# Kernel optimization log

Hardware: AMD Instinct MI355X
Metric: run time of the kernel (lower is better)

The kernel has to match this reference:

```python
import jax, jax.numpy as jnp
import numpy as np

K = 20  # rec list length

def _isin(a, b, bmask=None):
    # membership of each element of a in (masked) b; a,b are small [K] int arrays
    eq = a[:, None] == b[None, :]
    if bmask is not None:
        eq = eq & bmask[None, :]
    return eq.any(axis=1)

def _compact(vals, mask):
    # stable compaction of masked elements to the front, preserving order
    n = vals.shape[0]
    order = jnp.argsort(jnp.where(mask, jnp.arange(n), n))
    return vals[order], mask.sum()

def _fuse_one(top, mid, sim, probs, key):
    # greedy set-intersection fusion of three K-length rec lists (mirrors __fuse_rec_lists)
    m_tm = _isin(top, mid)
    m_ts = _isin(top, sim)
    m_ms = _isin(mid, sim)
    # faithful to the torch code's elementwise AND of masks over different lists
    mask_common = m_tm & m_ts & m_ms
    in_common_mid = _isin(mid, top, mask_common)
    mask_tm = m_tm & ~mask_common
    mask_ts = m_ts & ~mask_common
    mask_ms = m_ms & ~in_common_mid
    top_pool_m = ~mask_common & ~mask_tm & ~mask_ts
    mid_pool_m = ~in_common_mid & ~_isin(mid, top, mask_tm) & ~mask_ms
    sim_pool_m = (~_isin(sim, top, mask_common) & ~_isin(sim, top, mask_ts)
                  & ~_isin(sim, mid, mask_ms))
    det_vals = jnp.concatenate([top, top, top, mid])          # [4K]
    det_mask = jnp.concatenate([mask_common, mask_tm, mask_ts, mask_ms])
    det, n_det = _compact(det_vals, det_mask)
    pools, counts = jax.vmap(_compact)(
        jnp.stack([top, mid, sim]),
        jnp.stack([top_pool_m, mid_pool_m, sim_pool_m]))      # [3,K], [3]
    logp = jnp.log(probs)

    def step(carry, t):
        ptr, key = carry
        key, sub = jax.random.split(key)
        avail = ptr < counts
        idx = jax.random.categorical(sub, jnp.where(avail, logp, -jnp.inf))
        sampled = pools[idx, jnp.minimum(ptr[idx], K - 1)]
        use_det = t < n_det
        val = jnp.where(use_det, det[t], sampled)
        ptr = ptr.at[idx].add(jnp.where(use_det, 0, 1))
        return (ptr, key), val

    _, out = jax.lax.scan(step, (jnp.zeros(3, jnp.int32), key), jnp.arange(K))
    return out

def setup_inputs() -> dict:
    key = jax.random.key(0)
    ks = jax.random.split(key, 9)
    B, p_dim, latent = 2048, 64, 128
    n_users, n_items = 2000, 20000
    n_top, n_mid = 2000, 5000
    rng = np.random.default_rng(0)
    perm = rng.permutation(n_items)
    return {
        "X": jax.random.normal(ks[0], (B, p_dim), jnp.float32),
        "W_sp": jax.random.normal(ks[1], (p_dim, latent), jnp.float32) * 0.1,
        "W_sd": jax.random.normal(ks[2], (latent, n_top), jnp.float32) * 0.1,
        "W_mp": jax.random.normal(ks[3], (p_dim, latent), jnp.float32) * 0.1,
        "W_md": jax.random.normal(ks[4], (latent, n_mid), jnp.float32) * 0.1,
        "W_mapper": jax.random.normal(ks[5], (p_dim, 3), jnp.float32) * 0.1,
        "user_ratings": jax.random.uniform(ks[6], (n_users, n_items), jnp.float32),
        "user_personalities": jax.random.normal(ks[7], (n_users, p_dim), jnp.float32),
        "top_map": jnp.asarray(perm[:n_top], jnp.int32),
        "mid_map": jnp.asarray(perm[n_top:n_top + n_mid], jnp.int32),
    }

def reference(X, W_sp, W_sd, W_mp, W_md, W_mapper, user_ratings,
              user_personalities, top_map, mid_map):
    B = X.shape[0]
    n_items = user_ratings.shape[1]
    # small decoder path: prior -> dec -> scatter into full item space
    top_sub = (X @ W_sp) @ W_sd                                  # [B, n_top]
    top_full = jnp.zeros((B, n_items), X.dtype).at[:, top_map].set(top_sub)
    mid_sub = (X @ W_mp) @ W_md                                  # [B, n_mid]
    mid_full = jnp.zeros((B, n_items), X.dtype).at[:, mid_map].set(mid_sub)
    # personality-similarity recommendations
    sim_scores = (X @ user_personalities.T) @ user_ratings       # [B, n_items]
    top_idx = jax.lax.top_k(top_full, K)[1].astype(jnp.int32)
    mid_idx = jax.lax.top_k(mid_full, K)[1].astype(jnp.int32)
    sim_idx = jax.lax.top_k(sim_scores, K)[1].astype(jnp.int32)
    probs = jax.nn.softmax(X @ W_mapper, axis=-1)                # [B, 3]
    keys = jax.random.split(jax.random.key(42), B)
    out = jax.vmap(_fuse_one)(top_idx, mid_idx, sim_idx, probs, keys)
    return out.astype(jnp.float32)                               # [B, K]
```

## Files before the change

kernel.cpp:

```cpp
#include <hip/hip_runtime.h>
#include <stdint.h>
#include <math.h>

#define KK 20
#define RNG_PARTITIONABLE 1


__device__ __forceinline__ void tf2x32(uint32_t k0, uint32_t k1,
                                       uint32_t c0, uint32_t c1,
                                       uint32_t& o0, uint32_t& o1) {
  const uint32_t ks2 = k0 ^ k1 ^ 0x1BD11BDAu;
  uint32_t x0 = c0 + k0, x1 = c1 + k1;
#define ROTL32(x,d) (((x) << (d)) | ((x) >> (32 - (d))))
#define R4(ra,rb,rc,rd) \
  x0 += x1; x1 = ROTL32(x1, ra); x1 ^= x0; \
  x0 += x1; x1 = ROTL32(x1, rb); x1 ^= x0; \
  x0 += x1; x1 = ROTL32(x1, rc); x1 ^= x0; \
  x0 += x1; x1 = ROTL32(x1, rd); x1 ^= x0;
  R4(13,15,26,6);  x0 += k1;  x1 += ks2 + 1u;
  R4(17,29,16,24); x0 += ks2; x1 += k0 + 2u;
  R4(13,15,26,6);  x0 += k0;  x1 += k1 + 3u;
  R4(17,29,16,24); x0 += k1;  x1 += ks2 + 4u;
  R4(13,15,26,6);  x0 += ks2; x1 += k0 + 5u;
  o0 = x0; o1 = x1;
#undef R4
#undef ROTL32
}

__device__ __forceinline__ float u01_from_bits(uint32_t b) {
  float f = __uint_as_float((b >> 9) | 0x3f800000u) - 1.0f;
  return (f == 0.0f) ? 1.17549435e-38f : f;
}

#define GK 16

__global__ __launch_bounds__(256) void gemm_nn_k(
    const float* __restrict__ A, int lda,
    const float* __restrict__ Bg, int ldb,
    float* __restrict__ C, int ldc,
    int M, int N, int K, int kc) {
  __shared__ __align__(16) float As[GK][64 + 4];
  __shared__ __align__(16) float Bs[GK][128 + 4];
  const int tid = threadIdx.x;
  const int row0 = blockIdx.y * 64;
  const int col0 = blockIdx.x * 128;
  const int tr = tid >> 4, tc = tid & 15;
  const int kc_eff = (kc > 0) ? kc : K;
  float accM[4][8];
#pragma unroll
  for (int i = 0; i < 4; ++i)
#pragma unroll
    for (int j = 0; j < 8; ++j) accM[i][j] = 0.f;

  for (int c0 = 0; c0 < K; c0 += kc_eff) {
    const int kend = (c0 + kc_eff < K) ? (c0 + kc_eff) : K;
    float acc[4][8];
#pragma unroll
    for (int i = 0; i < 4; ++i)
#pragma unroll
      for (int j = 0; j < 8; ++j) acc[i][j] = 0.f;

    for (int k0 = c0; k0 < kend; k0 += GK) {
      {
        int ar = tid >> 2, ac = (tid & 3) << 2;
        int gr = row0 + ar, gc = k0 + ac;
        float4 v = make_float4(0.f, 0.f, 0.f, 0.f);
        if (gr < M) {
          if (gc + 3 < K) v = *(const float4*)(A + (size_t)gr * lda + gc);
          else {
            float t0 = (gc     < K) ? A[(size_t)gr * lda + gc]     : 0.f;
            float t1 = (gc + 1 < K) ? A[(size_t)gr * lda + gc + 1] : 0.f;
            float t2 = (gc + 2 < K) ? A[(size_t)gr * lda + gc + 2] : 0.f;
            float t3 = (gc + 3 < K) ? A[(size_t)gr * lda + gc + 3] : 0.f;
            v = make_float4(t0, t1, t2, t3);
          }
        }
        As[ac + 0][ar] = v.x; As[ac + 1][ar] = v.y;
        As[ac + 2][ar] = v.z; As[ac + 3][ar] = v.w;
      }
#pragma unroll
      for (int i = 0; i < 2; ++i) {
        int s = tid + i * 256;
        int br = s >> 5, bc = (s & 31) << 2;
        int gk = k0 + br, gc = col0 + bc;
        float4 v = make_float4(0.f, 0.f, 0.f, 0.f);
        if (gk < K) {
          if (gc + 3 < N) v = *(const float4*)(Bg + (size_t)gk * ldb + gc);
          else {
            float t0 = (gc     < N) ? Bg[(size_t)gk * ldb + gc]     : 0.f;
            float t1 = (gc + 1 < N) ? Bg[(size_t)gk * ldb + gc + 1] : 0.f;
            float t2 = (gc + 2 < N) ? Bg[(size_t)gk * ldb + gc + 2] : 0.f;
            float t3 = (gc + 3 < N) ? Bg[(size_t)gk * ldb + gc + 3] : 0.f;
            v = make_float4(t0, t1, t2, t3);
          }
        }
        *(float4*)&Bs[br][bc] = v;
      }
      __syncthreads();
#pragma unroll
      for (int kk = 0; kk < GK; ++kk) {
        float4 av = *(const float4*)&As[kk][tr << 2];
        float4 b0 = *(const float4*)&Bs[kk][tc << 2];
        float4 b1 = *(const float4*)&Bs[kk][64 + (tc << 2)];
        float a[4] = {av.x, av.y, av.z, av.w};
        float b[8] = {b0.x, b0.y, b0.z, b0.w, b1.x, b1.y, b1.z, b1.w};
#pragma unroll
        for (int i = 0; i < 4; ++i)
#pragma unroll
          for (int j = 0; j < 8; ++j)
            acc[i][j] = __fadd_rn(acc[i][j], __fmul_rn(a[i], b[j]));
      }
      __syncthreads();
    }
#pragma unroll
    for (int i = 0; i < 4; ++i)
#pragma unroll
      for (int j = 0; j < 8; ++j) accM[i][j] = __fadd_rn(accM[i][j], acc[i][j]);
  }
#pragma unroll
  for (int i = 0; i < 4; ++i) {
    int gr = row0 + (tr << 2) + i;
    if (gr >= M) continue;
#pragma unroll
    for (int j = 0; j < 8; ++j) {
      int gc = col0 + ((j < 4) ? (tc << 2) + j : 64 + (tc << 2) + (j - 4));
      if (gc < N) C[(size_t)gr * ldc + gc] = accM[i][j];
    }
  }
}

__global__ __launch_bounds__(256) void gemm_nt_k(
    const float* __restrict__ A, int lda,
    const float* __restrict__ Bg, int ldb,
    float* __restrict__ C, int ldc,
    int M, int N, int K) {
  __shared__ __align__(16) float As[16][128 + 4];
  __shared__ __align__(16) float Bs[16][128 + 4];
  const int tid = threadIdx.x;
  const int row0 = blockIdx.y * 128;
  const int col0 = blockIdx.x * 128;
  const int tr = tid >> 4, tc = tid & 15;
  float acc[8][8];
#pragma unroll
  for (int i = 0; i < 8; ++i)
#pragma unroll
    for (int j = 0; j < 8; ++j) acc[i][j] = 0.f;

  for (int k0 = 0; k0 < K; k0 += 16) {
#pragma unroll
    for (int i = 0; i < 2; ++i) {
      int s = tid + i * 256;
      int ar = s >> 2, ac = (s & 3) << 2;
      int gr = row0 + ar, gc = k0 + ac;
      float4 v = make_float4(0.f, 0.f, 0.f, 0.f);
      if (gr < M) {
        if (gc + 3 < K) v = *(const float4*)(A + (size_t)gr * lda + gc);
        else {
          float t0 = (gc     < K) ? A[(size_t)gr * lda + gc]     : 0.f;
          float t1 = (gc + 1 < K) ? A[(size_t)gr * lda + gc + 1] : 0.f;
          float t2 = (gc + 2 < K) ? A[(size_t)gr * lda + gc + 2] : 0.f;
          float t3 = (gc + 3 < K) ? A[(size_t)gr * lda + gc + 3] : 0.f;
          v = make_float4(t0, t1, t2, t3);
        }
      }
      As[ac + 0][ar] = v.x; As[ac + 1][ar] = v.y;
      As[ac + 2][ar] = v.z; As[ac + 3][ar] = v.w;
    }
#pragma unroll
    for (int i = 0; i < 2; ++i) {
      int s = tid + i * 256;
      int nr = s >> 2, kcc = (s & 3) << 2;
      int gn = col0 + nr, gk = k0 + kcc;
      float4 v = make_float4(0.f, 0.f, 0.f, 0.f);
      if (gn < N) {
        if (gk + 3 < K) v = *(const float4*)(Bg + (size_t)gn * ldb + gk);
        else {
          float t0 = (gk     < K) ? Bg[(size_t)gn * ldb + gk]     : 0.f;
          float t1 = (gk + 1 < K) ? Bg[(size_t)gn * ldb + gk + 1] : 0.f;
          float t2 = (gk + 2 < K) ? Bg[(size_t)gn * ldb + gk + 2] : 0.f;
          float t3 = (gk + 3 < K) ? Bg[(size_t)gn * ldb + gk + 3] : 0.f;
          v = make_float4(t0, t1, t2, t3);
        }
      }
      Bs[kcc + 0][nr] = v.x; Bs[kcc + 1][nr] = v.y;
      Bs[kcc + 2][nr] = v.z; Bs[kcc + 3][nr] = v.w;
    }
    __syncthreads();
#pragma unroll
    for (int kk = 0; kk < 16; ++kk) {
      float4 a0 = *(const float4*)&As[kk][tr * 8];
      float4 a1 = *(const float4*)&As[kk][tr * 8 + 4];
      float4 b0 = *(const float4*)&Bs[kk][tc * 8];
      float4 b1 = *(const float4*)&Bs[kk][tc * 8 + 4];
      float a[8] = {a0.x, a0.y, a0.z, a0.w, a1.x, a1.y, a1.z, a1.w};
      float b[8] = {b0.x, b0.y, b0.z, b0.w, b1.x, b1.y, b1.z, b1.w};
#pragma unroll
      for (int i = 0; i < 8; ++i)
#pragma unroll
        for (int j = 0; j < 8; ++j)
          acc[i][j] = __fadd_rn(acc[i][j], __fmul_rn(a[i], b[j]));
    }
    __syncthreads();
  }
#pragma unroll
  for (int i = 0; i < 8; ++i) {
    int gr = row0 + tr * 8 + i;
    if (gr >= M) continue;
#pragma unroll
    for (int j = 0; j < 8; ++j) {
      int gc = col0 + tc * 8 + j;
      if (gc < N) C[(size_t)gr * ldc + gc] = acc[i][j];
    }
  }
}

__global__ __launch_bounds__(256) void topk20_k(
    const float* __restrict__ mat, int ld, int ncols, int col_off,
    const int* __restrict__ map,
    float* __restrict__ sval, int* __restrict__ sidx, int merge) {
  __shared__ float shv[256][KK];
  __shared__ int   shi[256][KK];
  __shared__ float ov[KK];
  __shared__ int   oi[KK];
  const int r = blockIdx.x, t = threadIdx.x;
  const float* __restrict__ row = mat + (size_t)r * ld;
  float lv[KK]; int li[KK];
#pragma unroll
  for (int i = 0; i < KK; ++i) { lv[i] = -INFINITY; li[i] = 0x7fffffff; }
  for (int c = t; c < ncols; c += 256) {
    float v = row[c];
    if (v > lv[KK - 1]) {
      float cv = v; int ci = c;
#pragma unroll
      for (int i = 0; i < KK; ++i) {
        bool sw = cv > lv[i];
        float tv = lv[i]; int ti = li[i];
        lv[i] = sw ? cv : tv; li[i] = sw ? ci : ti;
        cv = sw ? tv : cv;    ci = sw ? ti : ci;
      }
    }
  }
#pragma unroll
  for (int i = 0; i < KK; ++i) { shv[t][i] = lv[i]; shi[t][i] = li[i]; }
  __syncthreads();
  if (t < 64) {
    int hp0 = 0, hp1 = 0, hp2 = 0, hp3 = 0;
    for (int round = 0; round < KK; ++round) {
      int base = t * 4;
      float v0 = (hp0 < KK) ? shv[base + 0][hp0] : -INFINITY;
      int   i0 = (hp0 < KK) ? shi[base + 0][hp0] : 0x7fffffff;
      float v1 = (hp1 < KK) ? shv[base + 1][hp1] : -INFINITY;
      int   i1 = (hp1 < KK) ? shi[base + 1][hp1] : 0x7fffffff;
      float v2 = (hp2 < KK) ? shv[base + 2][hp2] : -INFINITY;
      int   i2 = (hp2 < KK) ? shi[base + 2][hp2] : 0x7fffffff;
      float v3 = (hp3 < KK) ? shv[base + 3][hp3] : -INFINITY;
      int   i3 = (hp3 < KK) ? shi[base + 3][hp3] : 0x7fffffff;
      float bv = v0; int bi = i0; int bq = 0;
      if (v1 > bv || (v1 == bv && i1 < bi)) { bv = v1; bi = i1; bq = 1; }
      if (v2 > bv || (v2 == bv && i2 < bi)) { bv = v2; bi = i2; bq = 2; }
      if (v3 > bv || (v3 == bv && i3 < bi)) { bv = v3; bi = i3; bq = 3; }
      float cv = bv; int ci = bi; int cl = t; int cq = bq;
#pragma unroll
      for (int s2 = 1; s2 < 64; s2 <<= 1) {
        float vx = __shfl_xor(cv, s2);
        int   ix = __shfl_xor(ci, s2);
        int   lx = __shfl_xor(cl, s2);
        int   qx = __shfl_xor(cq, s2);
        if (vx > cv || (vx == cv && ix < ci)) { cv = vx; ci = ix; cl = lx; cq = qx; }
      }
      if (t == 0) { ov[round] = cv; oi[round] = ci; }
      if (cl == t) { hp0 += (cq == 0); hp1 += (cq == 1); hp2 += (cq == 2); hp3 += (cq == 3); }
    }
    if (t == 0) {
      float* SV = sval + (size_t)r * KK;
      int*   SI = sidx + (size_t)r * KK;
      if (!merge) {
        for (int i = 0; i < KK; ++i) {
          SV[i] = ov[i];
          SI[i] = map ? map[oi[i]] : (oi[i] + col_off);
        }
      } else {
        float mv[KK]; int mi[KK];
        int a = 0, b = 0;
        for (int i = 0; i < KK; ++i) {
          float va = SV[a]; int ia = SI[a];
          float vb = ov[b]; int ib = oi[b] + col_off;
          bool ta = (va > vb) || (va == vb && ia < ib);
          if (ta) { mv[i] = va; mi[i] = ia; ++a; }
          else    { mv[i] = vb; mi[i] = ib; ++b; }
        }
        for (int i = 0; i < KK; ++i) { SV[i] = mv[i]; SI[i] = mi[i]; }
      }
    }
  }
}

__global__ __launch_bounds__(256) void fuse_k(
    const float* __restrict__ X, const float* __restrict__ Wmap,
    const int* __restrict__ siT, const int* __restrict__ siM,
    const int* __restrict__ siS, float* __restrict__ out, int B) {
  int r = blockIdx.x * blockDim.x + threadIdx.x;
  if (r >= B) return;
  int top[KK], mid[KK], sim[KK];
  for (int i = 0; i < KK; ++i) {
    top[i] = siT[(size_t)r * KK + i];
    mid[i] = siM[(size_t)r * KK + i];
    sim[i] = siS[(size_t)r * KK + i];
  }
  float z0 = 0.f, z1 = 0.f, z2 = 0.f;
  for (int k = 0; k < 64; ++k) {
    float x = X[(size_t)r * 64 + k];
    z0 = __fadd_rn(z0, __fmul_rn(x, Wmap[k * 3 + 0]));
    z1 = __fadd_rn(z1, __fmul_rn(x, Wmap[k * 3 + 1]));
    z2 = __fadd_rn(z2, __fmul_rn(x, Wmap[k * 3 + 2]));
  }
  float zm = fmaxf(z0, fmaxf(z1, z2));
  float e0 = expf(z0 - zm), e1 = expf(z1 - zm), e2 = expf(z2 - zm);
  float s = __fadd_rn(__fadd_rn(e0, e1), e2);
  float logp[3] = { logf(__fdiv_rn(e0, s)), logf(__fdiv_rn(e1, s)), logf(__fdiv_rn(e2, s)) };
  bool m_tm[KK], m_ts[KK], m_ms[KK], maskC[KK], inCmid[KK], mTM[KK], mTS[KK], mMS[KK];
  for (int i = 0; i < KK; ++i) {
    bool a = false, b = false, c = false;
    for (int j = 0; j < KK; ++j) {
      a |= (top[i] == mid[j]);
      b |= (top[i] == sim[j]);
      c |= (mid[i] == sim[j]);
    }
    m_tm[i] = a; m_ts[i] = b; m_ms[i] = c;
  }
  for (int i = 0; i < KK; ++i) maskC[i] = m_tm[i] && m_ts[i] && m_ms[i];
  for (int i = 0; i < KK; ++i) {
    bool v = false;
    for (int j = 0; j < KK; ++j) v |= (mid[i] == top[j]) && maskC[j];
    inCmid[i] = v;
  }
  for (int i = 0; i < KK; ++i) {
    mTM[i] = m_tm[i] && !maskC[i];
    mTS[i] = m_ts[i] && !maskC[i];
    mMS[i] = m_ms[i] && !inCmid[i];
  }
  bool poolT[KK], poolM[KK], poolS[KK];
  for (int i = 0; i < KK; ++i) poolT[i] = !maskC[i] && !mTM[i] && !mTS[i];
  for (int i = 0; i < KK; ++i) {
    bool v = false;
    for (int j = 0; j < KK; ++j) v |= (mid[i] == top[j]) && mTM[j];
    poolM[i] = !inCmid[i] && !v && !mMS[i];
  }
  for (int i = 0; i < KK; ++i) {
    bool v1 = false, v2 = false, v3 = false;
    for (int j = 0; j < KK; ++j) {
      v1 |= (sim[i] == top[j]) && maskC[j];
      v2 |= (sim[i] == top[j]) && mTS[j];
      v3 |= (sim[i] == mid[j]) && mMS[j];
    }
    poolS[i] = !v1 && !v2 && !v3;
  }
  int det[KK]; int ndet = 0;
  for (int i = 0; i < KK; ++i) if (maskC[i]) { if (ndet < KK) det[ndet] = top[i]; ndet++; }
  for (int i = 0; i < KK; ++i) if (mTM[i])  { if (ndet < KK) det[ndet] = top[i]; ndet++; }
  for (int i = 0; i < KK; ++i) if (mTS[i])  { if (ndet < KK) det[ndet] = top[i]; ndet++; }
  for (int i = 0; i < KK; ++i) if (mMS[i])  { if (ndet < KK) det[ndet] = mid[i]; ndet++; }
  int pool[3][KK]; int cnt[3];
  {
    int c = 0;
    for (int i = 0; i < KK; ++i) if (poolT[i]) pool[0][c++] = top[i];
    cnt[0] = c;
    for (int i = 0; i < KK; ++i) if (!poolT[i]) pool[0][c++] = top[i];
  }
  {
    int c = 0;
    for (int i = 0; i < KK; ++i) if (poolM[i]) pool[1][c++] = mid[i];
    cnt[1] = c;
    for (int i = 0; i < KK; ++i) if (!poolM[i]) pool[1][c++] = mid[i];
  }
  {
    int c = 0;
    for (int i = 0; i < KK; ++i) if (poolS[i]) pool[2][c++] = sim[i];
    cnt[2] = c;
    for (int i = 0; i < KK; ++i) if (!poolS[i]) pool[2][c++] = sim[i];
  }
  uint32_t k0, k1;
#if RNG_PARTITIONABLE
  { uint32_t a, b; tf2x32(0u, 42u, 0u, (uint32_t)r, a, b); k0 = a; k1 = b; }
#else
  {
    if (r < 1024) {
      uint32_t x0, x1, y0, y1;
      tf2x32(0u, 42u, (uint32_t)(2 * r),     (uint32_t)(2048 + 2 * r),     x0, x1);
      tf2x32(0u, 42u, (uint32_t)(2 * r + 1), (uint32_t)(2048 + 2 * r + 1), y0, y1);
      k0 = x0; k1 = y0;
    } else {
      int j = 2 * r - 2048;
      uint32_t x0, x1, y0, y1;
      tf2x32(0u, 42u, (uint32_t)j,       (uint32_t)(2048 + j),     x0, x1);
      tf2x32(0u, 42u, (uint32_t)(j + 1), (uint32_t)(2048 + j + 1), y0, y1);
      k0 = x1; k1 = y1;
    }
  }
#endif
  int ptr0 = 0, ptr1 = 0, ptr2 = 0;
  for (int t = 0; t < KK; ++t) {
    uint32_t nk0, nk1, sb0, sb1;
#if RNG_PARTITIONABLE
    tf2x32(k0, k1, 0u, 0u, nk0, nk1);
    tf2x32(k0, k1, 0u, 1u, sb0, sb1);
#else
    { uint32_t p0x, p0y, p1x, p1y;
      tf2x32(k0, k1, 0u, 2u, p0x, p0y);
      tf2x32(k0, k1, 1u, 3u, p1x, p1y);
      nk0 = p0x; nk1 = p1x; sb0 = p0y; sb1 = p1y; }
#endif
    k0 = nk0; k1 = nk1;
    float g[3];
#if RNG_PARTITIONABLE
    for (int i = 0; i < 3; ++i) {
      uint32_t a, b; tf2x32(sb0, sb1, 0u, (uint32_t)i, a, b);
      float u = u01_from_bits(a ^ b);
      g[i] = -logf(-logf(u));
    }
#else
    { uint32_t q0x, q0y, q1x, q1y;
      tf2x32(sb0, sb1, 0u, 2u, q0x, q0y);
      tf2x32(sb0, sb1, 1u, 0u, q1x, q1y);
      uint32_t bits[3] = { q0x, q1x, q0y };
      for (int i = 0; i < 3; ++i) {
        float u = u01_from_bits(bits[i]);
        g[i] = -logf(-logf(u));
      }
    }
#endif
    float s0 = (ptr0 < cnt[0]) ? g[0] + logp[0] : -INFINITY;
    float s1 = (ptr1 < cnt[1]) ? g[1] + logp[1] : -INFINITY;
    float s2 = (ptr2 < cnt[2]) ? g[2] + logp[2] : -INFINITY;
    int idx = 0; float best = s0;
    if (s1 > best) { best = s1; idx = 1; }
    if (s2 > best) { best = s2; idx = 2; }
    int p = (idx == 0) ? ptr0 : ((idx == 1) ? ptr1 : ptr2);
    int sampled = pool[idx][p < (KK - 1) ? p : (KK - 1)];
    int val = (t < ndet) ? det[t] : sampled;
    out[(size_t)r * KK + t] = (float)val;
    if (t >= ndet) { if (idx == 0) ++ptr0; else if (idx == 1) ++ptr1; else ++ptr2; }
  }
}

extern "C" void kernel_launch(void* const* d_in, const int* in_sizes, int n_in,
                              void* d_out, int out_size, void* d_ws, size_t ws_size,
                              hipStream_t stream) {
  const float* X    = (const float*)d_in[0];
  const float* Wsp  = (const float*)d_in[1];
  const float* Wsd  = (const float*)d_in[2];
  const float* Wmp  = (const float*)d_in[3];
  const float* Wmd  = (const float*)d_in[4];
  const float* Wmap = (const float*)d_in[5];
  const float* R    = (const float*)d_in[6];
  const float* U    = (const float*)d_in[7];
  const int* top_map = (const int*)d_in[8];
  const int* mid_map = (const int*)d_in[9];
  float* out = (float*)d_out;

  const int B = 2048, P_DIM = 64, LAT = 128;
  const int N_TOP = 2000, N_MID = 5000, N_USERS = 2000;
  const int CHUNK = 5000, N_CHUNKS = 4;
  const int KC_EIGEN = 320;

  char* ws = (char*)d_ws;
  size_t off = 0;
  auto alloc = [&](size_t bytes) -> void* {
    off = (off + 255) & ~(size_t)255;
    void* p = ws + off; off += bytes; return p;
  };
  float* H   = (float*)alloc((size_t)B * LAT * 4);
  float* Pm  = (float*)alloc((size_t)B * N_USERS * 4);
  float* CH  = (float*)alloc((size_t)B * CHUNK * 4);
  float* svT = (float*)alloc((size_t)B * KK * 4);
  int*   siT = (int*)  alloc((size_t)B * KK * 4);
  float* svM = (float*)alloc((size_t)B * KK * 4);
  int*   siM = (int*)  alloc((size_t)B * KK * 4);
  float* svS = (float*)alloc((size_t)B * KK * 4);
  int*   siS = (int*)  alloc((size_t)B * KK * 4);
  (void)ws_size; (void)in_sizes; (void)n_in; (void)out_size;

  dim3 blk(256);
  gemm_nn_k<<<dim3(1, 32), blk, 0, stream>>>(X, P_DIM, Wsp, LAT, H, LAT, B, LAT, P_DIM, 0);
  gemm_nn_k<<<dim3(16, 32), blk, 0, stream>>>(H, LAT, Wsd, N_TOP, CH, N_TOP, B, N_TOP, LAT, 0);
  topk20_k<<<dim3(B), blk, 0, stream>>>(CH, N_TOP, N_TOP, 0, top_map, svT, siT, 0);
  gemm_nn_k<<<dim3(1, 32), blk, 0, stream>>>(X, P_DIM, Wmp, LAT, H, LAT, B, LAT, P_DIM, 0);
  gemm_nn_k<<<dim3(40, 32), blk, 0, stream>>>(H, LAT, Wmd, N_MID, CH, N_MID, B, N_MID, LAT, 0);
  topk20_k<<<dim3(B), blk, 0, stream>>>(CH, N_MID, N_MID, 0, mid_map, svM, siM, 0);
  gemm_nt_k<<<dim3(16, 16), blk, 0, stream>>>(X, P_DIM, U, P_DIM, Pm, N_USERS, B, N_USERS, P_DIM);
  for (int c = 0; c < N_CHUNKS; ++c) {
    gemm_nn_k<<<dim3(40, 32), blk, 0, stream>>>(Pm, N_USERS, R + (size_t)c * CHUNK, 20000,
                                                CH, CHUNK, B, CHUNK, N_USERS, KC_EIGEN);
    topk20_k<<<dim3(B), blk, 0, stream>>>(CH, CHUNK, CHUNK, c * CHUNK, nullptr, svS, siS, c ? 1 : 0);
  }
  fuse_k<<<dim3(B / 256), blk, 0, stream>>>(X, Wmap, siT, siM, siS, out, B);
}
```

Measured before the change: 3.430 ms.

## Prefetch GEMM tiles into registers, deepen k-tile, merge top-k launches, unchunk sim

The fp32 GEMM now uses 32-deep k-tiles and loads the next tile from global memory into registers while the current one is computed from shared memory, to hide load latency. When the workspace is large enough, the top and mid top-k passes run as one two-row-grid launch. The similarity GEMM and its top-k then run once over all 20000 items instead of four chunks with a merge step. This trades extra workspace, a larger 20000-column scratch matrix and more registers and shared memory per block (which may lower occupancy) for fewer launches and more parallel work per launch.

```diff
diff --git a/kernel.cpp b/kernel.cpp
--- a/kernel.cpp
+++ b/kernel.cpp
@@ -32,20 +32,77 @@
   return (f == 0.0f) ? 1.17549435e-38f : f;
 }
 
-#define GK 16
+#define BK 32
 
 __global__ __launch_bounds__(256) void gemm_nn_k(
     const float* __restrict__ A, int lda,
     const float* __restrict__ Bg, int ldb,
     float* __restrict__ C, int ldc,
     int M, int N, int K, int kc) {
-  __shared__ __align__(16) float As[GK][64 + 4];
-  __shared__ __align__(16) float Bs[GK][128 + 4];
+  __shared__ __align__(16) float As[BK][64 + 4];
+  __shared__ __align__(16) float Bs[BK][128 + 4];
   const int tid = threadIdx.x;
   const int row0 = blockIdx.y * 64;
   const int col0 = blockIdx.x * 128;
   const int tr = tid >> 4, tc = tid & 15;
   const int kc_eff = (kc > 0) ? kc : K;
+
+  const int a_ar0 = tid >> 3,        a_ac0 = (tid & 7) << 2;
+  const int a_ar1 = (tid + 256) >> 3, a_ac1 = ((tid + 256) & 7) << 2;
+  int b_br[4], b_bc[4];
+#pragma unroll
+  for (int i = 0; i < 4; ++i) { int s = tid + i * 256; b_br[i] = s >> 5; b_bc[i] = (s & 31) << 2; }
+
+  float4 pa0, pa1, pb[4];
+  auto load_tile = [&](int k0) {
+    {
+      int gr = row0 + a_ar0, gc = k0 + a_ac0;
+      float4 v = make_float4(0.f, 0.f, 0.f, 0.f);
+      if (gr < M) {
+        if (gc + 3 < K) v = *(const float4*)(A + (size_t)gr * lda + gc);
+        else {
+          float t0 = (gc     < K) ? A[(size_t)gr * lda + gc]     : 0.f;
+          float t1 = (gc + 1 < K) ? A[(size_t)gr * lda + gc + 1] : 0.f;
+          float t2 = (gc + 2 < K) ? A[(size_t)gr * lda + gc + 2] : 0.f;
+          float t3 = (gc + 3 < K) ? A[(size_t)gr * lda + gc + 3] : 0.f;
+          v = make_float4(t0, t1, t2, t3);
+        }
+      }
+      pa0 = v;
+    }
+    {
+      int gr = row0 + a_ar1, gc = k0 + a_ac1;
+      float4 v = make_float4(0.f, 0.f, 0.f, 0.f);
+      if (gr < M) {
+        if (gc + 3 < K) v = *(const float4*)(A + (size_t)gr * lda + gc);
+        else {
+          float t0 = (gc     < K) ? A[(size_t)gr * lda + gc]     : 0.f;
+          float t1 = (gc + 1 < K) ? A[(size_t)gr * lda + gc + 1] : 0.f;
+          float t2 = (gc + 2 < K) ? A[(size_t)gr * lda + gc + 2] : 0.f;
+          float t3 = (gc + 3 < K) ? A[(size_t)gr * lda + gc + 3] : 0.f;
+          v = make_float4(t0, t1, t2, t3);
+        }
+      }
+      pa1 = v;
+    }
+#pragma unroll
+    for (int i = 0; i < 4; ++i) {
+      int gk = k0 + b_br[i], gc = col0 + b_bc[i];
+      float4 v = make_float4(0.f, 0.f, 0.f, 0.f);
+      if (gk < K) {
+        if (gc + 3 < N) v = *(const float4*)(Bg + (size_t)gk * ldb + gc);
+        else {
+          float t0 = (gc     < N) ? Bg[(size_t)gk * ldb + gc]     : 0.f;
+          float t1 = (gc + 1 < N) ? Bg[(size_t)gk * ldb + gc + 1] : 0.f;
+          float t2 = (gc + 2 < N) ? Bg[(size_t)gk * ldb + gc + 2] : 0.f;
+          float t3 = (gc + 3 < N) ? Bg[(size_t)gk * ldb + gc + 3] : 0.f;
+          v = make_float4(t0, t1, t2, t3);
+        }
+      }
+      pb[i] = v;
+    }
+  };
+
   float accM[4][8];
 #pragma unroll
   for (int i = 0; i < 4; ++i)
@@ -60,45 +117,18 @@
 #pragma unroll
       for (int j = 0; j < 8; ++j) acc[i][j] = 0.f;
 
-    for (int k0 = c0; k0 < kend; k0 += GK) {
-      {
-        int ar = tid >> 2, ac = (tid & 3) << 2;
-        int gr = row0 + ar, gc = k0 + ac;
-        float4 v = make_float4(0.f, 0.f, 0.f, 0.f);
-        if (gr < M) {
-          if (gc + 3 < K) v = *(const float4*)(A + (size_t)gr * lda + gc);
-          else {
-            float t0 = (gc     < K) ? A[(size_t)gr * lda + gc]     : 0.f;
-            float t1 = (gc + 1 < K) ? A[(size_t)gr * lda + gc + 1] : 0.f;
-            float t2 = (gc + 2 < K) ? A[(size_t)gr * lda + gc + 2] : 0.f;
-            float t3 = (gc + 3 < K) ? A[(size_t)gr * lda + gc + 3] : 0.f;
-            v = make_float4(t0, t1, t2, t3);
-          }
-        }
-        As[ac + 0][ar] = v.x; As[ac + 1][ar] = v.y;
-        As[ac + 2][ar] = v.z; As[ac + 3][ar] = v.w;
-      }
-#pragma unroll
-      for (int i = 0; i < 2; ++i) {
-        int s = tid + i * 256;
-        int br = s >> 5, bc = (s & 31) << 2;
-        int gk = k0 + br, gc = col0 + bc;
-        float4 v = make_float4(0.f, 0.f, 0.f, 0.f);
-        if (gk < K) {
-          if (gc + 3 < N) v = *(const float4*)(Bg + (size_t)gk * ldb + gc);
-          else {
-            float t0 = (gc     < N) ? Bg[(size_t)gk * ldb + gc]     : 0.f;
-            float t1 = (gc + 1 < N) ? Bg[(size_t)gk * ldb + gc + 1] : 0.f;
-            float t2 = (gc + 2 < N) ? Bg[(size_t)gk * ldb + gc + 2] : 0.f;
-            float t3 = (gc + 3 < N) ? Bg[(size_t)gk * ldb + gc + 3] : 0.f;
-            v = make_float4(t0, t1, t2, t3);
-          }
-        }
-        *(float4*)&Bs[br][bc] = v;
-      }
+    load_tile(c0);
+    for (int k0 = c0; k0 < kend; k0 += BK) {
+      As[a_ac0 + 0][a_ar0] = pa0.x; As[a_ac0 + 1][a_ar0] = pa0.y;
+      As[a_ac0 + 2][a_ar0] = pa0.z; As[a_ac0 + 3][a_ar0] = pa0.w;
+      As[a_ac1 + 0][a_ar1] = pa1.x; As[a_ac1 + 1][a_ar1] = pa1.y;
+      As[a_ac1 + 2][a_ar1] = pa1.z; As[a_ac1 + 3][a_ar1] = pa1.w;
+#pragma unroll
+      for (int i = 0; i < 4; ++i) *(float4*)&Bs[b_br[i]][b_bc[i]] = pb[i];
       __syncthreads();
-#pragma unroll
-      for (int kk = 0; kk < GK; ++kk) {
+      if (k0 + BK < kend) load_tile(k0 + BK);
+      const int klim = (kend - k0 < BK) ? (kend - k0) : BK;
+      for (int kk = 0; kk < klim; ++kk) {
         float4 av = *(const float4*)&As[kk][tr << 2];
         float4 b0 = *(const float4*)&Bs[kk][tc << 2];
         float4 b1 = *(const float4*)&Bs[kk][64 + (tc << 2)];
@@ -214,16 +244,12 @@
   }
 }
 
-__global__ __launch_bounds__(256) void topk20_k(
-    const float* __restrict__ mat, int ld, int ncols, int col_off,
+__device__ __forceinline__ void topk20_row(
+    const float* __restrict__ row, int ncols, int col_off,
     const int* __restrict__ map,
-    float* __restrict__ sval, int* __restrict__ sidx, int merge) {
-  __shared__ float shv[256][KK];
-  __shared__ int   shi[256][KK];
-  __shared__ float ov[KK];
-  __shared__ int   oi[KK];
-  const int r = blockIdx.x, t = threadIdx.x;
-  const float* __restrict__ row = mat + (size_t)r * ld;
+    float* __restrict__ SV, int* __restrict__ SI, int merge,
+    float (*shv)[KK], int (*shi)[KK], float* ov, int* oi) {
+  const int t = threadIdx.x;
   float lv[KK]; int li[KK];
 #pragma unroll
   for (int i = 0; i < KK; ++i) { lv[i] = -INFINITY; li[i] = 0x7fffffff; }
@@ -272,8 +298,6 @@
       if (cl == t) { hp0 += (cq == 0); hp1 += (cq == 1); hp2 += (cq == 2); hp3 += (cq == 3); }
     }
     if (t == 0) {
-      float* SV = sval + (size_t)r * KK;
-      int*   SI = sidx + (size_t)r * KK;
       if (!merge) {
         for (int i = 0; i < KK; ++i) {
           SV[i] = ov[i];
@@ -293,6 +317,37 @@
       }
     }
   }
+}
+
+__global__ __launch_bounds__(256) void topk20_k(
+    const float* __restrict__ mat, int ld, int ncols, int col_off,
+    const int* __restrict__ map,
+    float* __restrict__ sval, int* __restrict__ sidx, int merge) {
+  __shared__ float shv[256][KK];
+  __shared__ int   shi[256][KK];
+  __shared__ float ov[KK];
+  __shared__ int   oi[KK];
+  const int r = blockIdx.x;
+  topk20_row(mat + (size_t)r * ld, ncols, col_off, map,
+             sval + (size_t)r * KK, sidx + (size_t)r * KK, merge, shv, shi, ov, oi);
+}
+
+__global__ __launch_bounds__(256) void topk20_dual_k(
+    const float* __restrict__ m0, int nc0, const int* __restrict__ map0,
+    float* __restrict__ sv0, int* __restrict__ si0,
+    const float* __restrict__ m1, int nc1, const int* __restrict__ map1,
+    float* __restrict__ sv1, int* __restrict__ si1) {
+  __shared__ float shv[256][KK];
+  __shared__ int   shi[256][KK];
+  __shared__ float ov[KK];
+  __shared__ int   oi[KK];
+  const int r = blockIdx.x;
+  if (blockIdx.y == 0)
+    topk20_row(m0 + (size_t)r * nc0, nc0, 0, map0,
+               sv0 + (size_t)r * KK, si0 + (size_t)r * KK, 0, shv, shi, ov, oi);
+  else
+    topk20_row(m1 + (size_t)r * nc1, nc1, 0, map1,
+               sv1 + (size_t)r * KK, si1 + (size_t)r * KK, 0, shv, shi, ov, oi);
 }
 
 __global__ __launch_bounds__(256) void fuse_k(
@@ -459,9 +514,9 @@
   float* out = (float*)d_out;
 
   const int B = 2048, P_DIM = 64, LAT = 128;
-  const int N_TOP = 2000, N_MID = 5000, N_USERS = 2000;
-  const int CHUNK = 5000, N_CHUNKS = 4;
+  const int N_TOP = 2000, N_MID = 5000, N_USERS = 2000, N_ITEMS = 20000;
   const int KC_EIGEN = 320;
+  (void)in_sizes; (void)n_in; (void)out_size;
 
   char* ws = (char*)d_ws;
   size_t off = 0;
@@ -469,29 +524,61 @@
     off = (off + 255) & ~(size_t)255;
     void* p = ws + off; off += bytes; return p;
   };
-  float* H   = (float*)alloc((size_t)B * LAT * 4);
-  float* Pm  = (float*)alloc((size_t)B * N_USERS * 4);
-  float* CH  = (float*)alloc((size_t)B * CHUNK * 4);
-  float* svT = (float*)alloc((size_t)B * KK * 4);
-  int*   siT = (int*)  alloc((size_t)B * KK * 4);
-  float* svM = (float*)alloc((size_t)B * KK * 4);
-  int*   siM = (int*)  alloc((size_t)B * KK * 4);
-  float* svS = (float*)alloc((size_t)B * KK * 4);
-  int*   siS = (int*)  alloc((size_t)B * KK * 4);
-  (void)ws_size; (void)in_sizes; (void)n_in; (void)out_size;
+
+  const size_t BIG_NEED = (size_t)B * (2 * LAT + N_USERS + N_TOP + N_MID + N_ITEMS + 6 * KK) * 4
+                          + 16 * 256;
+  const bool big = (ws_size >= BIG_NEED);
 
   dim3 blk(256);
-  gemm_nn_k<<<dim3(1, 32), blk, 0, stream>>>(X, P_DIM, Wsp, LAT, H, LAT, B, LAT, P_DIM, 0);
-  gemm_nn_k<<<dim3(16, 32), blk, 0, stream>>>(H, LAT, Wsd, N_TOP, CH, N_TOP, B, N_TOP, LAT, 0);
-  topk20_k<<<dim3(B), blk, 0, stream>>>(CH, N_TOP, N_TOP, 0, top_map, svT, siT, 0);
-  gemm_nn_k<<<dim3(1, 32), blk, 0, stream>>>(X, P_DIM, Wmp, LAT, H, LAT, B, LAT, P_DIM, 0);
-  gemm_nn_k<<<dim3(40, 32), blk, 0, stream>>>(H, LAT, Wmd, N_MID, CH, N_MID, B, N_MID, LAT, 0);
-  topk20_k<<<dim3(B), blk, 0, stream>>>(CH, N_MID, N_MID, 0, mid_map, svM, siM, 0);
-  gemm_nt_k<<<dim3(16, 16), blk, 0, stream>>>(X, P_DIM, U, P_DIM, Pm, N_USERS, B, N_USERS, P_DIM);
-  for (int c = 0; c < N_CHUNKS; ++c) {
-    gemm_nn_k<<<dim3(40, 32), blk, 0, stream>>>(Pm, N_USERS, R + (size_t)c * CHUNK, 20000,
-                                                CH, CHUNK, B, CHUNK, N_USERS, KC_EIGEN);
-    topk20_k<<<dim3(B), blk, 0, stream>>>(CH, CHUNK, CHUNK, c * CHUNK, nullptr, svS, siS, c ? 1 : 0);
-  }
-  fuse_k<<<dim3(B / 256), blk, 0, stream>>>(X, Wmap, siT, siM, siS, out, B);
-}
+  if (big) {
+    float* Ht  = (float*)alloc((size_t)B * LAT * 4);
+    float* Hm  = (float*)alloc((size_t)B * LAT * 4);
+    float* Pm  = (float*)alloc((size_t)B * N_USERS * 4);
+    float* CHt = (float*)alloc((size_t)B * N_TOP * 4);
+    float* CHm = (float*)alloc((size_t)B * N_MID * 4);
+    float* CHs = (float*)alloc((size_t)B * N_ITEMS * 4);
+    float* svT = (float*)alloc((size_t)B * KK * 4);
+    int*   siT = (int*)  alloc((size_t)B * KK * 4);
+    float* svM = (float*)alloc((size_t)B * KK * 4);
+    int*   siM = (int*)  alloc((size_t)B * KK * 4);
+    float* svS = (float*)alloc((size_t)B * KK * 4);
+    int*   siS = (int*)  alloc((size_t)B * KK * 4);
+
+    gemm_nn_k<<<dim3(1, 32), blk, 0, stream>>>(X, P_DIM, Wsp, LAT, Ht, LAT, B, LAT, P_DIM, 0);
+    gemm_nn_k<<<dim3(1, 32), blk, 0, stream>>>(X, P_DIM, Wmp, LAT, Hm, LAT, B, LAT, P_DIM, 0);
+    gemm_nn_k<<<dim3(16, 32), blk, 0, stream>>>(Ht, LAT, Wsd, N_TOP, CHt, N_TOP, B, N_TOP, LAT, 0);
+    gemm_nn_k<<<dim3(40, 32), blk, 0, stream>>>(Hm, LAT, Wmd, N_MID, CHm, N_MID, B, N_MID, LAT, 0);
+    topk20_dual_k<<<dim3(B, 2), blk, 0, stream>>>(CHt, N_TOP, top_map, svT, siT,
+                                                  CHm, N_MID, mid_map, svM, siM);
+    gemm_nt_k<<<dim3(16, 16), blk, 0, stream>>>(X, P_DIM, U, P_DIM, Pm, N_USERS, B, N_USERS, P_DIM);
+    gemm_nn_k<<<dim3(157, 32), blk, 0, stream>>>(Pm, N_USERS, R, N_ITEMS,
+                                                 CHs, N_ITEMS, B, N_ITEMS, N_USERS, KC_EIGEN);
+    topk20_k<<<dim3(B), blk, 0, stream>>>(CHs, N_ITEMS, N_ITEMS, 0, nullptr, svS, siS, 0);
+    fuse_k<<<dim3(B / 256), blk, 0, stream>>>(X, Wmap, siT, siM, siS, out, B);
+  } else {
+    const int CHUNK = 5000, N_CHUNKS = 4;
+    float* H   = (float*)alloc((size_t)B * LAT * 4);
+    float* Pm  = (float*)alloc((size_t)B * N_USERS * 4);
+    float* CH  = (float*)alloc((size_t)B * CHUNK * 4);
+    float* svT = (float*)alloc((size_t)B * KK * 4);
+    int*   siT = (int*)  alloc((size_t)B * KK * 4);
+    float* svM = (float*)alloc((size_t)B * KK * 4);
+    int*   siM = (int*)  alloc((size_t)B * KK * 4);
+    float* svS = (float*)alloc((size_t)B * KK * 4);
+    int*   siS = (int*)  alloc((size_t)B * KK * 4);
+
+    gemm_nn_k<<<dim3(1, 32), blk, 0, stream>>>(X, P_DIM, Wsp, LAT, H, LAT, B, LAT, P_DIM, 0);
+    gemm_nn_k<<<dim3(16, 32), blk, 0, stream>>>(H, LAT, Wsd, N_TOP, CH, N_TOP, B, N_TOP, LAT, 0);
+    topk20_k<<<dim3(B), blk, 0, stream>>>(CH, N_TOP, N_TOP, 0, top_map, svT, siT, 0);
+    gemm_nn_k<<<dim3(1, 32), blk, 0, stream>>>(X, P_DIM, Wmp, LAT, H, LAT, B, LAT, P_DIM, 0);
+    gemm_nn_k<<<dim3(40, 32), blk, 0, stream>>>(H, LAT, Wmd, N_MID, CH, N_MID, B, N_MID, LAT, 0);
+    topk20_k<<<dim3(B), blk, 0, stream>>>(CH, N_MID, N_MID, 0, mid_map, svM, siM, 0);
+    gemm_nt_k<<<dim3(16, 16), blk, 0, stream>>>(X, P_DIM, U, P_DIM, Pm, N_USERS, B, N_USERS, P_DIM);
+    for (int c = 0; c < N_CHUNKS; ++c) {
+      gemm_nn_k<<<dim3(40, 32), blk, 0, stream>>>(Pm, N_USERS, R + (size_t)c * CHUNK, N_ITEMS,
+                                                  CH, CHUNK, B, CHUNK, N_USERS, KC_EIGEN);
+      topk20_k<<<dim3(B), blk, 0, stream>>>(CH, CHUNK, CHUNK, c * CHUNK, nullptr, svS, siS, c ? 1 : 0);
+    }
+    fuse_k<<<dim3(B / 256), blk, 0, stream>>>(X, Wmap, siT, siM, siS, out, B);
+  }
+}
```

Measured after the change: 3.669 ms. 1.07x slower.
